# Optimization experiments

Hardware: AMD Instinct MI355X
Metric: run time of the kernel (lower is better)

Reference implementation:

```python
import jax, jax.numpy as jnp
import numpy as np

BITS = 4
GROUPSIZE = 128
IN_FEATURES = 4096
OUT_FEATURES = 11008
N_TOKENS = 4096
MAXQ = (1 << BITS) - 1  # 15
PACK = 32 // BITS       # 8 values per int32


def setup_inputs() -> dict:
    key = jax.random.key(0)
    k1, k2, k3, k4, k5 = jax.random.split(key, 5)
    x = jax.random.normal(k1, (N_TOKENS, IN_FEATURES), dtype=jnp.float16)
    # packed 4-bit weights: random int32 bit patterns -> random nibbles
    qweight = jax.random.randint(k2, (IN_FEATURES // 32 * BITS, OUT_FEATURES),
                                 jnp.iinfo(jnp.int32).min, jnp.iinfo(jnp.int32).max,
                                 dtype=jnp.int32)
    n_groups = IN_FEATURES // GROUPSIZE
    qzeros = jax.random.randint(k3, (n_groups, OUT_FEATURES // 32 * BITS),
                                jnp.iinfo(jnp.int32).min, jnp.iinfo(jnp.int32).max,
                                dtype=jnp.int32)
    # small positive scales, as produced by GPTQ quantization
    scales = (jax.random.uniform(k4, (n_groups, OUT_FEATURES), dtype=jnp.float32) * 0.01 + 0.005).astype(jnp.float16)
    g_idx = (jnp.arange(IN_FEATURES) // GROUPSIZE).astype(jnp.int32)
    bias = jax.random.normal(k5, (OUT_FEATURES,), dtype=jnp.float16)
    return {"x": x, "qweight": qweight, "qzeros": qzeros,
            "scales": scales, "g_idx": g_idx, "bias": bias}


def _dequantize(qweight, qzeros, scales, g_idx):
    # nibble shift offsets 0,4,...,28
    shifts = jnp.arange(0, 32, BITS, dtype=jnp.int32)
    # unpack zeros: [G, out//8] -> [G, out//8, 8] -> [G, out]; GPTQ stores zero-1
    zeros = ((qzeros[:, :, None] >> shifts[None, None, :]) & MAXQ) + 1
    zeros = zeros.reshape(scales.shape)  # [G, out]
    # unpack weights: [in//8, out] -> [in//8, 8, out] -> [in, out]
    w_int = (qweight[:, None, :] >> shifts[None, :, None]) & MAXQ
    w_int = w_int.reshape(IN_FEATURES, OUT_FEATURES)
    # dequantize: scales[g] * (w - zeros[g]), fp16 like the torch path
    w = scales[g_idx] * (w_int - zeros[g_idx]).astype(scales.dtype)  # [in, out]
    return w


def reference(x, qweight, qzeros, scales, g_idx, bias):
    w = _dequantize(qweight, qzeros, scales, g_idx)
    out = jnp.matmul(x, w) + bias  # [N_TOKENS, out]
    return out
```

## Files before the change

### kernel.cpp

```cpp
#include <hip/hip_runtime.h>


#define TM 4096
#define TK 4096
#define TN 11008
#define GS 128
#define NG (TK / GS)
#define QZC (TN / 8)

#define BM2 256
#define BN2 256
#define BK2 64
#define NKT (TK / BK2)
#define NBN (TN / BN2)
#define GRID2 ((TM / BM2) * (TN / BN2))

#define BM 128
#define BN 128
#define BK 32

#define XB_BYTES ((size_t)TM * TK * 2)
#define WT_BYTES ((size_t)TN * TK * 2)
#define WS_NEED  (XB_BYTES + WT_BYTES)

typedef __attribute__((ext_vector_type(8))) short short8;
typedef __attribute__((ext_vector_type(4))) float floatx4;

union S8U { short8 v; unsigned u[4]; };

__device__ __forceinline__ unsigned short f2bf_rn(float f) {
    unsigned u = __builtin_bit_cast(unsigned, f);
    u += 0x7FFFu + ((u >> 16) & 1u);
    return (unsigned short)(u >> 16);
}
__device__ __forceinline__ unsigned pack2(float a, float b) {
    return (unsigned)f2bf_rn(a) | ((unsigned)f2bf_rn(b) << 16);
}

__global__ __launch_bounds__(256)
void conv_x(const float* __restrict__ X, unsigned short* __restrict__ Xb)
{
    const size_t i = ((size_t)blockIdx.x * 256 + threadIdx.x) * 8;
    floatx4 v0 = *(const floatx4*)(X + i);
    floatx4 v1 = *(const floatx4*)(X + i + 4);
    S8U o;
    o.u[0] = pack2(v0[0], v0[1]); o.u[1] = pack2(v0[2], v0[3]);
    o.u[2] = pack2(v1[0], v1[1]); o.u[3] = pack2(v1[2], v1[3]);
    *(short8*)(Xb + i) = o.v;
}

__global__ __launch_bounds__(256)
void dequant_w(const int* __restrict__ QW, const int* __restrict__ QZ,
               const float* __restrict__ SC, unsigned short* __restrict__ Wt)
{
    const int ptile = blockIdx.x % 32;
    const int ntile = blockIdx.x / 32;
    const int g  = ptile;
    const int p  = ptile * 16 + (threadIdx.x & 15);
    const int nb = threadIdx.x >> 4;

    #pragma unroll
    for (int i = 0; i < 4; ++i) {
        const int n = ntile * 64 + nb + 16 * i;
        const float s = SC[(size_t)g * TN + n];
        const int z = (int)(((unsigned)QZ[g * QZC + (n >> 3)] >> ((n & 7) * 4)) & 15u) + 1;
        const float zc = -s * (float)z;
        const unsigned q = (unsigned)QW[(size_t)p * TN + n];
        const unsigned qe = q & 0x0F0F0F0Fu;
        const unsigned qo = (q >> 4) & 0x0F0F0F0Fu;
        S8U vv;
        #pragma unroll
        for (int jj = 0; jj < 4; ++jj) {
            const float w0 = (float)((qe >> (8 * jj)) & 0xFFu);
            const float w1 = (float)((qo >> (8 * jj)) & 0xFFu);
            vv.u[jj] = pack2(fmaf(w0, s, zc), fmaf(w1, s, zc));
        }
        *(short8*)(Wt + (size_t)n * TK + p * 8) = vv.v;
    }
}

#define GLDS(gp, lp) __builtin_amdgcn_global_load_lds( \
    (const __attribute__((address_space(1))) void*)(gp), \
    (__attribute__((address_space(3))) void*)(lp), 16, 0, 0)

#define STAGE(op, gptr, buf, half, kt) do {                                   \
    const unsigned short* _g = (gptr) + (size_t)(half) * 128 * TK             \
                                      + (size_t)(kt) * BK2;                   \
    short* _l = &sh[buf][op][(half) * 8192 + ldst];                           \
    GLDS(_g, _l);                                                             \
    GLDS(_g + (size_t)64 * TK, _l + 4096);                                    \
} while (0)

#define RDA(buf, mi, ks) (*(const short8*)&sh[buf][0][ \
    (wr * 128 + (mi) * 16 + l16) * 64 + ((((ks) << 2) | quad) ^ swz) * 8])
#define RDB(buf, ni, ks) (*(const short8*)&sh[buf][1][ \
    (wc * 64 + (ni) * 16 + l16) * 64 + ((((ks) << 2) | quad) ^ swz) * 8])

#define BARRIER __builtin_amdgcn_s_barrier()
#define LGKM0 do { asm volatile("s_waitcnt lgkmcnt(0)" ::: "memory");         \
                   __builtin_amdgcn_sched_barrier(0); } while (0)
#define VMW4  asm volatile("s_waitcnt vmcnt(4)" ::: "memory")

template<int MI0, int NI0>
__device__ __forceinline__ void mfma_quad(floatx4 (&acc)[8][4],
                                          const short8 (&a)[4][2],
                                          const short8 (&b)[4][2]) {
    __builtin_amdgcn_s_setprio(1);
    #pragma unroll
    for (int m = 0; m < 4; ++m)
        #pragma unroll
        for (int n = 0; n < 2; ++n)
            #pragma unroll
            for (int ks = 0; ks < 2; ++ks)
                acc[MI0 + m][NI0 + n] = __builtin_amdgcn_mfma_f32_16x16x32_bf16(
                    a[m][ks], b[NI0 + n][ks], acc[MI0 + m][NI0 + n], 0, 0, 0);
    __builtin_amdgcn_s_setprio(0);
}

__global__ __launch_bounds__(512, 2)
void gemm_8ph(const unsigned short* __restrict__ A,
              const unsigned short* __restrict__ Bt,
              const float* __restrict__ BIAS,
              float* __restrict__ OUT)
{
    __shared__ __align__(16) short sh[2][2][BM2 * BK2];

    const int tid  = threadIdx.x;
    const int lane = tid & 63;
    const int wave = tid >> 6;
    const int wr   = wave >> 2;
    const int wc   = wave & 3;
    const int quad = lane >> 4;
    const int l16  = lane & 15;
    const int swz  = l16 & 7;

    const int bid  = blockIdx.x;
    const int wgid = (bid & 7) * (GRID2 / 8) + (bid >> 3);
    const int bm = wgid / NBN;
    const int bn = wgid % NBN;

    const int srow = wave * 8 + (lane >> 3);
    const int scol = 8 * ((lane & 7) ^ (lane >> 3));
    const unsigned short* Ag = A  + (size_t)(bm * BM2 + srow) * TK + scol;
    const unsigned short* Bg = Bt + (size_t)(bn * BN2 + srow) * TK + scol;
    const int ldst = wave * 512 + lane * 8;

    floatx4 acc[8][4];
    #pragma unroll
    for (int i = 0; i < 8; ++i)
        #pragma unroll
        for (int j = 0; j < 4; ++j)
            acc[i][j] = (floatx4){0.f, 0.f, 0.f, 0.f};

    short8 a[4][2], b[4][2];

    STAGE(0, Ag, 0, 0, 0); STAGE(0, Ag, 0, 1, 0);
    STAGE(1, Bg, 0, 0, 0); STAGE(1, Bg, 0, 1, 0);
    STAGE(1, Bg, 1, 0, 1); STAGE(1, Bg, 1, 1, 1);
    VMW4;
    BARRIER;

    for (int it = 0; it < NKT / 2; ++it) {
        const int t  = 2 * it;
        const int t2 = (t + 2 < NKT) ? t + 2 : NKT - 1;
        const int t3 = (t + 3 < NKT) ? t + 3 : NKT - 1;

        #pragma unroll
        for (int m = 0; m < 4; ++m) { a[m][0] = RDA(0, m, 0); a[m][1] = RDA(0, m, 1); }
        #pragma unroll
        for (int n = 0; n < 2; ++n) { b[n][0] = RDB(0, n, 0); b[n][1] = RDB(0, n, 1); }
        STAGE(0, Ag, 1, 0, t + 1);
        BARRIER; LGKM0;
        mfma_quad<0, 0>(acc, a, b);
        BARRIER;

        #pragma unroll
        for (int n = 2; n < 4; ++n) { b[n][0] = RDB(0, n, 0); b[n][1] = RDB(0, n, 1); }
        STAGE(0, Ag, 1, 1, t + 1);
        BARRIER; LGKM0;
        mfma_quad<0, 2>(acc, a, b);
        BARRIER;

        #pragma unroll
        for (int m = 0; m < 4; ++m) { a[m][0] = RDA(0, m + 4, 0); a[m][1] = RDA(0, m + 4, 1); }
        STAGE(1, Bg, 0, 0, t2);
        BARRIER; LGKM0;
        mfma_quad<4, 0>(acc, a, b);
        BARRIER;

        STAGE(1, Bg, 0, 1, t2);
        VMW4;
        BARRIER;
        mfma_quad<4, 2>(acc, a, b);
        BARRIER;

        #pragma unroll
        for (int m = 0; m < 4; ++m) { a[m][0] = RDA(1, m, 0); a[m][1] = RDA(1, m, 1); }
        #pragma unroll
        for (int n = 0; n < 2; ++n) { b[n][0] = RDB(1, n, 0); b[n][1] = RDB(1, n, 1); }
        STAGE(0, Ag, 0, 0, t2);
        BARRIER; LGKM0;
        mfma_quad<0, 0>(acc, a, b);
        BARRIER;

        #pragma unroll
        for (int n = 2; n < 4; ++n) { b[n][0] = RDB(1, n, 0); b[n][1] = RDB(1, n, 1); }
        STAGE(0, Ag, 0, 1, t2);
        BARRIER; LGKM0;
        mfma_quad<0, 2>(acc, a, b);
        BARRIER;

        #pragma unroll
        for (int m = 0; m < 4; ++m) { a[m][0] = RDA(1, m + 4, 0); a[m][1] = RDA(1, m + 4, 1); }
        STAGE(1, Bg, 1, 0, t3);
        BARRIER; LGKM0;
        mfma_quad<4, 0>(acc, a, b);
        BARRIER;

        STAGE(1, Bg, 1, 1, t3);
        VMW4;
        BARRIER;
        mfma_quad<4, 2>(acc, a, b);
        BARRIER;
    }

    const int row0 = bm * BM2 + wr * 128 + quad * 4;
    const int col0 = bn * BN2 + wc * 64 + l16;
    #pragma unroll
    for (int ni = 0; ni < 4; ++ni) {
        const int col = col0 + ni * 16;
        const float bv = BIAS[col];
        #pragma unroll
        for (int mi = 0; mi < 8; ++mi) {
            #pragma unroll
            for (int r = 0; r < 4; ++r) {
                const int row = row0 + mi * 16 + r;
                OUT[(size_t)row * TN + col] = acc[mi][ni][r] + bv;
            }
        }
    }
}

__global__ __launch_bounds__(256)
void gemm_fused_fallback(const float* __restrict__ X, const int* __restrict__ QW,
                         const int* __restrict__ QZ, const float* __restrict__ SC,
                         const float* __restrict__ BIAS, float* __restrict__ OUT)
{
    __shared__ __align__(16) short As[BM * BK];
    __shared__ __align__(16) short Bs[BN * BK];

    const int tid  = threadIdx.x;
    const int lane = tid & 63;
    const int wave = tid >> 6;
    const int bm = blockIdx.x / (TN / BN);
    const int bn = blockIdx.x % (TN / BN);
    const int wm = (wave & 1) * 64;
    const int wn = (wave >> 1) * 64;
    const int quad = lane >> 4;
    const int l16  = lane & 15;

    const int a_r = tid >> 2;
    const int a_c = (tid & 3) * 8;
    const float* agp = X + (size_t)(bm * BM + a_r) * TK + a_c;
    short* alp = As + a_r * BK + a_c;

    const int b_n = tid & 127;
    const int b_p = tid >> 7;
    const int n_g = bn * BN + b_n;
    const int zsh = (n_g & 7) * 4;

    floatx4 acc[4][4];
    #pragma unroll
    for (int i = 0; i < 4; ++i)
        #pragma unroll
        for (int j = 0; j < 4; ++j)
            acc[i][j] = (floatx4){0.f, 0.f, 0.f, 0.f};

    for (int g = 0; g < NG; ++g) {
        const float s = SC[(size_t)g * TN + n_g];
        const int z = (int)(((unsigned)QZ[g * QZC + (n_g >> 3)] >> zsh) & 15u) + 1;
        const float zc = -s * (float)z;

        #pragma unroll
        for (int t = 0; t < GS / BK; ++t) {
            const int k0 = g * GS + t * BK;
            floatx4 v0 = *(const floatx4*)(agp + k0);
            floatx4 v1 = *(const floatx4*)(agp + k0 + 4);
            floatx4 v2 = *(const floatx4*)(agp + (size_t)64 * TK + k0);
            floatx4 v3 = *(const floatx4*)(agp + (size_t)64 * TK + k0 + 4);
            const unsigned q0 = (unsigned)QW[(size_t)(k0 / 8 + b_p)     * TN + n_g];
            const unsigned q1 = (unsigned)QW[(size_t)(k0 / 8 + b_p + 2) * TN + n_g];

            S8U aw0, aw1;
            aw0.u[0] = pack2(v0[0], v0[1]); aw0.u[1] = pack2(v0[2], v0[3]);
            aw0.u[2] = pack2(v1[0], v1[1]); aw0.u[3] = pack2(v1[2], v1[3]);
            aw1.u[0] = pack2(v2[0], v2[1]); aw1.u[1] = pack2(v2[2], v2[3]);
            aw1.u[2] = pack2(v3[0], v3[1]); aw1.u[3] = pack2(v3[2], v3[3]);
            *(short8*)alp = aw0.v;
            *(short8*)(alp + 64 * BK) = aw1.v;

            const unsigned qs[2] = {q0, q1};
            #pragma unroll
            for (int i = 0; i < 2; ++i) {
                const int p = b_p + i * 2;
                const unsigned q = qs[i];
                const unsigned qe = q & 0x0F0F0F0Fu;
                const unsigned qo = (q >> 4) & 0x0F0F0F0Fu;
                S8U vv;
                #pragma unroll
                for (int jj = 0; jj < 4; ++jj) {
                    const float w0 = (float)((qe >> (8 * jj)) & 0xFFu);
                    const float w1 = (float)((qo >> (8 * jj)) & 0xFFu);
                    vv.u[jj] = pack2(fmaf(w0, s, zc), fmaf(w1, s, zc));
                }
                *(short8*)(Bs + b_n * BK + p * 8) = vv.v;
            }

            __syncthreads();
            short8 af[4], bfr[4];
            #pragma unroll
            for (int i = 0; i < 4; ++i) {
                af[i]  = *(const short8*)(As + (wm + i * 16 + l16) * BK + quad * 8);
                bfr[i] = *(const short8*)(Bs + (wn + i * 16 + l16) * BK + quad * 8);
            }
            #pragma unroll
            for (int mi = 0; mi < 4; ++mi)
                #pragma unroll
                for (int ni = 0; ni < 4; ++ni)
                    acc[mi][ni] = __builtin_amdgcn_mfma_f32_16x16x32_bf16(
                        af[mi], bfr[ni], acc[mi][ni], 0, 0, 0);
            __syncthreads();
        }
    }

    const int col0 = bn * BN + wn + l16;
    const int row0 = bm * BM + wm + quad * 4;
    #pragma unroll
    for (int ni = 0; ni < 4; ++ni) {
        const int col = col0 + ni * 16;
        const float bv = BIAS[col];
        #pragma unroll
        for (int mi = 0; mi < 4; ++mi) {
            #pragma unroll
            for (int r = 0; r < 4; ++r) {
                const int row = row0 + mi * 16 + r;
                OUT[(size_t)row * TN + col] = acc[mi][ni][r] + bv;
            }
        }
    }
}

extern "C" void kernel_launch(void* const* d_in, const int* in_sizes, int n_in,
                              void* d_out, int out_size, void* d_ws, size_t ws_size,
                              hipStream_t stream) {
    const void* px = nullptr; const void* pqw = nullptr; const void* pqz = nullptr;
    const void* psc = nullptr; const void* pbi = nullptr;
    for (int i = 0; i < n_in; ++i) {
        switch (in_sizes[i]) {
            case 16777216: px  = d_in[i]; break;
            case 5636096:  pqw = d_in[i]; break;
            case 352256:   psc = d_in[i]; break;
            case 44032:    pqz = d_in[i]; break;
            case 11008:    pbi = d_in[i]; break;
            default: break;
        }
    }
    if (!px)  px  = d_in[0];
    if (!pqw) pqw = d_in[1];
    if (!pqz) pqz = d_in[2];
    if (!psc) psc = d_in[3];
    if (!pbi) pbi = d_in[5];

    if (ws_size >= WS_NEED) {
        unsigned short* Xb = (unsigned short*)d_ws;
        unsigned short* Wt = (unsigned short*)((char*)d_ws + XB_BYTES);

        conv_x<<<dim3(TM * TK / 8 / 256), 256, 0, stream>>>((const float*)px, Xb);
        dequant_w<<<dim3(32 * (TN / 64)), 256, 0, stream>>>(
            (const int*)pqw, (const int*)pqz, (const float*)psc, Wt);
        gemm_8ph<<<dim3(GRID2), 512, 0, stream>>>(
            Xb, Wt, (const float*)pbi, (float*)d_out);
    } else {
        gemm_fused_fallback<<<dim3((TM / BM) * (TN / BN)), 256, 0, stream>>>(
            (const float*)px, (const int*)pqw, (const int*)pqz,
            (const float*)psc, (const float*)pbi, (float*)d_out);
    }
}
```

Baseline: 574.9 us.

## Merge prep kernels and software-pipeline LDS fragment reads with MFMA

Combines the x-to-bf16 conversion and weight dequantization into a single launch, removing one kernel launch and the gap between the two. In the GEMM main loop, A and B fragment registers are split into separate double sets so the LDS reads for the next sub-tile are issued before the current MFMA block rather than waited on with lgkmcnt(0). The LDS read latency can then hide behind matrix math, and the explicit barrier/wait pairs before each MFMA group are removed. This raises register pressure from the extra fragment buffers and relies on compiler-inserted waits for correctness.

```diff
diff --git a/kernel.cpp b/kernel.cpp
--- a/kernel.cpp
+++ b/kernel.cpp
@@ -15,6 +15,9 @@
 #define NBN (TN / BN2)
 #define GRID2 ((TM / BM2) * (TN / BN2))
 
+#define DQB (32 * (TN / 64))
+#define CVB (TM * TK / 8 / 256)
+
 #define BM 128
 #define BN 128
 #define BK 32
@@ -38,44 +41,44 @@
 }
 
 __global__ __launch_bounds__(256)
-void conv_x(const float* __restrict__ X, unsigned short* __restrict__ Xb)
+void prep(const float* __restrict__ X, unsigned short* __restrict__ Xb,
+          const int* __restrict__ QW, const int* __restrict__ QZ,
+          const float* __restrict__ SC, unsigned short* __restrict__ Wt)
 {
-    const size_t i = ((size_t)blockIdx.x * 256 + threadIdx.x) * 8;
-    floatx4 v0 = *(const floatx4*)(X + i);
-    floatx4 v1 = *(const floatx4*)(X + i + 4);
-    S8U o;
-    o.u[0] = pack2(v0[0], v0[1]); o.u[1] = pack2(v0[2], v0[3]);
-    o.u[2] = pack2(v1[0], v1[1]); o.u[3] = pack2(v1[2], v1[3]);
-    *(short8*)(Xb + i) = o.v;
-}
-
-__global__ __launch_bounds__(256)
-void dequant_w(const int* __restrict__ QW, const int* __restrict__ QZ,
-               const float* __restrict__ SC, unsigned short* __restrict__ Wt)
-{
-    const int ptile = blockIdx.x % 32;
-    const int ntile = blockIdx.x / 32;
-    const int g  = ptile;
-    const int p  = ptile * 16 + (threadIdx.x & 15);
-    const int nb = threadIdx.x >> 4;
-
-    #pragma unroll
-    for (int i = 0; i < 4; ++i) {
-        const int n = ntile * 64 + nb + 16 * i;
-        const float s = SC[(size_t)g * TN + n];
-        const int z = (int)(((unsigned)QZ[g * QZC + (n >> 3)] >> ((n & 7) * 4)) & 15u) + 1;
-        const float zc = -s * (float)z;
-        const unsigned q = (unsigned)QW[(size_t)p * TN + n];
-        const unsigned qe = q & 0x0F0F0F0Fu;
-        const unsigned qo = (q >> 4) & 0x0F0F0F0Fu;
-        S8U vv;
-        #pragma unroll
-        for (int jj = 0; jj < 4; ++jj) {
-            const float w0 = (float)((qe >> (8 * jj)) & 0xFFu);
-            const float w1 = (float)((qo >> (8 * jj)) & 0xFFu);
-            vv.u[jj] = pack2(fmaf(w0, s, zc), fmaf(w1, s, zc));
-        }
-        *(short8*)(Wt + (size_t)n * TK + p * 8) = vv.v;
+    if (blockIdx.x < DQB) {
+        const int ptile = blockIdx.x % 32;
+        const int ntile = blockIdx.x / 32;
+        const int g  = ptile;
+        const int p  = ptile * 16 + (threadIdx.x & 15);
+        const int nb = threadIdx.x >> 4;
+
+        #pragma unroll
+        for (int i = 0; i < 4; ++i) {
+            const int n = ntile * 64 + nb + 16 * i;
+            const float s = SC[(size_t)g * TN + n];
+            const int z = (int)(((unsigned)QZ[g * QZC + (n >> 3)] >> ((n & 7) * 4)) & 15u) + 1;
+            const float zc = -s * (float)z;
+            const unsigned q = (unsigned)QW[(size_t)p * TN + n];
+            const unsigned qe = q & 0x0F0F0F0Fu;
+            const unsigned qo = (q >> 4) & 0x0F0F0F0Fu;
+            S8U vv;
+            #pragma unroll
+            for (int jj = 0; jj < 4; ++jj) {
+                const float w0 = (float)((qe >> (8 * jj)) & 0xFFu);
+                const float w1 = (float)((qo >> (8 * jj)) & 0xFFu);
+                vv.u[jj] = pack2(fmaf(w0, s, zc), fmaf(w1, s, zc));
+            }
+            *(short8*)(Wt + (size_t)n * TK + p * 8) = vv.v;
+        }
+    } else {
+        const size_t bid = blockIdx.x - DQB;
+        const size_t i = (bid * 256 + threadIdx.x) * 8;
+        floatx4 v0 = *(const floatx4*)(X + i);
+        floatx4 v1 = *(const floatx4*)(X + i + 4);
+        S8U o;
+        o.u[0] = pack2(v0[0], v0[1]); o.u[1] = pack2(v0[2], v0[3]);
+        o.u[2] = pack2(v1[0], v1[1]); o.u[3] = pack2(v1[2], v1[3]);
+        *(short8*)(Xb + i) = o.v;
     }
 }
 
@@ -96,15 +99,27 @@
 #define RDB(buf, ni, ks) (*(const short8*)&sh[buf][1][ \
     (wc * 64 + (ni) * 16 + l16) * 64 + ((((ks) << 2) | quad) ^ swz) * 8])
 
+#define RD_A4(dst, buf, mi0) do {                                             \
+    _Pragma("unroll")                                                         \
+    for (int _m = 0; _m < 4; ++_m) {                                          \
+        dst[_m][0] = RDA(buf, (mi0) + _m, 0);                                 \
+        dst[_m][1] = RDA(buf, (mi0) + _m, 1);                                 \
+    } } while (0)
+#define RD_B2(dst, buf, ni0) do {                                             \
+    _Pragma("unroll")                                                         \
+    for (int _n = 0; _n < 2; ++_n) {                                          \
+        dst[_n][0] = RDB(buf, (ni0) + _n, 0);                                 \
+        dst[_n][1] = RDB(buf, (ni0) + _n, 1);                                 \
+    } } while (0)
+
 #define BARRIER __builtin_amdgcn_s_barrier()
-#define LGKM0 do { asm volatile("s_waitcnt lgkmcnt(0)" ::: "memory");         \
-                   __builtin_amdgcn_sched_barrier(0); } while (0)
-#define VMW4  asm volatile("s_waitcnt vmcnt(4)" ::: "memory")
+#define SB0     __builtin_amdgcn_sched_barrier(0)
+#define VMW4    asm volatile("s_waitcnt vmcnt(4)" ::: "memory")
 
 template<int MI0, int NI0>
-__device__ __forceinline__ void mfma_quad(floatx4 (&acc)[8][4],
-                                          const short8 (&a)[4][2],
-                                          const short8 (&b)[4][2]) {
+__device__ __forceinline__ void mfma_q(floatx4 (&acc)[8][4],
+                                       const short8 (&a)[4][2],
+                                       const short8 (&b)[2][2]) {
     __builtin_amdgcn_s_setprio(1);
     #pragma unroll
     for (int m = 0; m < 4; ++m)
@@ -113,7 +128,7 @@
             #pragma unroll
             for (int ks = 0; ks < 2; ++ks)
                 acc[MI0 + m][NI0 + n] = __builtin_amdgcn_mfma_f32_16x16x32_bf16(
-                    a[m][ks], b[NI0 + n][ks], acc[MI0 + m][NI0 + n], 0, 0, 0);
+                    a[m][ks], b[n][ks], acc[MI0 + m][NI0 + n], 0, 0, 0);
     __builtin_amdgcn_s_setprio(0);
 }
 
@@ -152,75 +167,60 @@
         for (int j = 0; j < 4; ++j)
             acc[i][j] = (floatx4){0.f, 0.f, 0.f, 0.f};
 
-    short8 a[4][2], b[4][2];
+    short8 a03[4][2], a47[4][2], b01[2][2], b23[2][2];
 
     STAGE(0, Ag, 0, 0, 0); STAGE(0, Ag, 0, 1, 0);
     STAGE(1, Bg, 0, 0, 0); STAGE(1, Bg, 0, 1, 0);
     STAGE(1, Bg, 1, 0, 1); STAGE(1, Bg, 1, 1, 1);
     VMW4;
-    BARRIER;
+    BARRIER; SB0;
+    RD_A4(a03, 0, 0); RD_B2(b01, 0, 0);
 
     for (int it = 0; it < NKT / 2; ++it) {
         const int t  = 2 * it;
         const int t2 = (t + 2 < NKT) ? t + 2 : NKT - 1;
         const int t3 = (t + 3 < NKT) ? t + 3 : NKT - 1;
 
-        #pragma unroll
-        for (int m = 0; m < 4; ++m) { a[m][0] = RDA(0, m, 0); a[m][1] = RDA(0, m, 1); }
-        #pragma unroll
-        for (int n = 0; n < 2; ++n) { b[n][0] = RDB(0, n, 0); b[n][1] = RDB(0, n, 1); }
         STAGE(0, Ag, 1, 0, t + 1);
-        BARRIER; LGKM0;
-        mfma_quad<0, 0>(acc, a, b);
-        BARRIER;
-
-        #pragma unroll
-        for (int n = 2; n < 4; ++n) { b[n][0] = RDB(0, n, 0); b[n][1] = RDB(0, n, 1); }
+        RD_B2(b23, 0, 2);
+        mfma_q<0, 0>(acc, a03, b01);
+        BARRIER;
+
         STAGE(0, Ag, 1, 1, t + 1);
-        BARRIER; LGKM0;
-        mfma_quad<0, 2>(acc, a, b);
-        BARRIER;
-
-        #pragma unroll
-        for (int m = 0; m < 4; ++m) { a[m][0] = RDA(0, m + 4, 0); a[m][1] = RDA(0, m + 4, 1); }
+        RD_A4(a47, 0, 4);
+        mfma_q<0, 2>(acc, a03, b23);
+        BARRIER;
+
         STAGE(1, Bg, 0, 0, t2);
-        BARRIER; LGKM0;
-        mfma_quad<4, 0>(acc, a, b);
+        mfma_q<4, 0>(acc, a47, b01);
         BARRIER;
 
         STAGE(1, Bg, 0, 1, t2);
         VMW4;
-        BARRIER;
-        mfma_quad<4, 2>(acc, a, b);
-        BARRIER;
-
-        #pragma unroll
-        for (int m = 0; m < 4; ++m) { a[m][0] = RDA(1, m, 0); a[m][1] = RDA(1, m, 1); }
-        #pragma unroll
-        for (int n = 0; n < 2; ++n) { b[n][0] = RDB(1, n, 0); b[n][1] = RDB(1, n, 1); }
+        BARRIER; SB0;
+        RD_A4(a03, 1, 0); RD_B2(b01, 1, 0);
+        mfma_q<4, 2>(acc, a47, b23);
+        BARRIER;
+
         STAGE(0, Ag, 0, 0, t2);
-        BARRIER; LGKM0;
-        mfma_quad<0, 0>(acc, a, b);
-        BARRIER;
-
-        #pragma unroll
-        for (int n = 2; n < 4; ++n) { b[n][0] = RDB(1, n, 0); b[n][1] = RDB(1, n, 1); }
+        RD_B2(b23, 1, 2);
+        mfma_q<0, 0>(acc, a03, b01);
+        BARRIER;
+
         STAGE(0, Ag, 0, 1, t2);
-        BARRIER; LGKM0;
-        mfma_quad<0, 2>(acc, a, b);
-        BARRIER;
-
-        #pragma unroll
-        for (int m = 0; m < 4; ++m) { a[m][0] = RDA(1, m + 4, 0); a[m][1] = RDA(1, m + 4, 1); }
+        RD_A4(a47, 1, 4);
+        mfma_q<0, 2>(acc, a03, b23);
+        BARRIER;
+
         STAGE(1, Bg, 1, 0, t3);
-        BARRIER; LGKM0;
-        mfma_quad<4, 0>(acc, a, b);
+        mfma_q<4, 0>(acc, a47, b01);
         BARRIER;
 
         STAGE(1, Bg, 1, 1, t3);
         VMW4;
-        BARRIER;
-        mfma_quad<4, 2>(acc, a, b);
+        BARRIER; SB0;
+        RD_A4(a03, 0, 0); RD_B2(b01, 0, 0);
+        mfma_q<4, 2>(acc, a47, b23);
         BARRIER;
     }
 
@@ -375,9 +375,9 @@
         unsigned short* Xb = (unsigned short*)d_ws;
         unsigned short* Wt = (unsigned short*)((char*)d_ws + XB_BYTES);
 
-        conv_x<<<dim3(TM * TK / 8 / 256), 256, 0, stream>>>((const float*)px, Xb);
-        dequant_w<<<dim3(32 * (TN / 64)), 256, 0, stream>>>(
-            (const int*)pqw, (const int*)pqz, (const float*)psc, Wt);
+        prep<<<dim3(DQB + CVB), 256, 0, stream>>>(
+            (const float*)px, Xb, (const int*)pqw, (const int*)pqz,
+            (const float*)psc, Wt);
         gemm_8ph<<<dim3(GRID2), 512, 0, stream>>>(
             Xb, Wt, (const float*)pbi, (float*)d_out);
     } else {
```

Measured after the change: 999.0 us. 73.8% more time.
